# Kernel tuning notes

Measured on AMD Instinct MI355X. Metric: run time of the kernel, lower is better.

The kernel has to match this reference:

```python
import jax, jax.numpy as jnp
import numpy as np

KS = (10, 25, 50, 100)  # numbers of highest-scored tiles to average (eval mode averages over all)
CLAMP = 1e4


def setup_inputs() -> dict:
    key = jax.random.key(0)
    k1, k2, k3, k4, k5, k6, k7 = jax.random.split(key, 7)
    B, C, N, H, O = 8, 2048, 8000, 256, 1000
    x = jax.random.normal(k1, (B, C, N), dtype=jnp.float32)
    # Conv1d(kernel=1) weights == [out, in] matrices
    W0 = jax.random.normal(k2, (H, C), dtype=jnp.float32) * (1.0 / np.sqrt(C))
    b0 = jax.random.normal(k3, (H,), dtype=jnp.float32) * 0.01
    W1 = jax.random.normal(k4, (H, H), dtype=jnp.float32) * (1.0 / np.sqrt(H))
    b1 = jax.random.normal(k5, (H,), dtype=jnp.float32) * 0.01
    W2 = jax.random.normal(k6, (O, H), dtype=jnp.float32) * (1.0 / np.sqrt(H))
    b2 = jax.random.normal(k7, (O,), dtype=jnp.float32) * 0.01
    return {"x": x, "W0": W0, "b0": b0, "W1": W1, "b1": b1, "W2": W2, "b2": b2}


def reference(x, W0, b0, W1, b1, W2, b2):
    # x: [B, C, N] tile features. Eval-mode dropout is identity.
    # mask: tile is 'real' if its max feature > 0 (padding tiles are all-zero)
    mask = (jnp.max(x, axis=1, keepdims=True) > 0).astype(x.dtype)  # [B,1,N]
    # 1x1 conv stack (Conv1d kernel=1 == per-tile matmul)
    h = jnp.einsum('hc,bcn->bhn', W0, x) + b0[None, :, None]
    h = jnp.clip(jax.nn.relu(h), -CLAMP, CLAMP)
    h = jnp.einsum('hg,bgn->bhn', W1, h) + b1[None, :, None]
    h = jnp.clip(jax.nn.relu(h), -CLAMP, CLAMP)
    y = jnp.einsum('oh,bhn->bon', W2, h) + b2[None, :, None]  # [B,O,N]
    y = y * mask
    # top-kmax once (sorted descending); top-k for smaller k is a prefix slice
    kmax = max(KS)
    t, _ = jax.lax.top_k(y, kmax)  # [B,O,kmax]
    pred = jnp.zeros(y.shape[:2], dtype=y.dtype)  # [B,O]
    inv = 1.0 / len(KS)
    for k in KS:
        num = jnp.sum(t[:, :, :k] * mask[:, :, :k], axis=2)  # [B,O]
        den = jnp.sum(mask[:, :, :k], axis=2)                 # [B,1]
        pred = pred + (num / den) * inv
    return pred
```

## Files before the change

### kernel.cpp

```cpp
#include <hip/hip_runtime.h>
#include <hip/hip_bf16.h>
#include <stdint.h>

typedef __bf16 bf16;
typedef __bf16 bf16x8 __attribute__((ext_vector_type(8)));
typedef __bf16 bf16x4 __attribute__((ext_vector_type(4)));
typedef float  floatx4 __attribute__((ext_vector_type(4)));
typedef unsigned int uint32;

#define B_  8
#define C_  2048
#define N_  8000
#define H_  256
#define O_  1000
#define OP_ 1024

__device__ __forceinline__ void gll16(const void* g, void* l) {
  __builtin_amdgcn_global_load_lds((const __attribute__((address_space(1))) void*)g,
                                   (__attribute__((address_space(3))) void*)l, 16, 0, 0);
}

__global__ __launch_bounds__(256) void castw(const float* __restrict__ W0,
                                             const float* __restrict__ W1,
                                             const float* __restrict__ W2,
                                             bf16* __restrict__ W0b,
                                             bf16* __restrict__ W1b,
                                             bf16* __restrict__ W2b) {
  int idx = blockIdx.x * 256 + threadIdx.x;
  if (idx < 524288) {
    W0b[idx] = (bf16)W0[idx];
  } else if (idx < 524288 + 65536) {
    int i = idx - 524288;
    W1b[i] = (bf16)W1[i];
  } else {
    int i = idx - (524288 + 65536);
    int o = i >> 8, k = i & 255;
    W2b[i] = (o < O_) ? (bf16)W2[o * 256 + k] : (bf16)0.0f;
  }
}

__global__ __launch_bounds__(256) void gemm1(const float* __restrict__ x,
                                             const bf16* __restrict__ W0b,
                                             const float* __restrict__ bias0,
                                             bf16* __restrict__ h1T,
                                             float* __restrict__ maskb) {
  __shared__ union {
    struct { bf16 A[H_ * 32]; bf16 Bt[64 * 40]; } st;
    bf16 HT[64 * 264];
  } sm;
  __shared__ float sbias[256];
  __shared__ uint32 nflag[64];

  const int tid  = threadIdx.x;
  const int wave = tid >> 6, lane = tid & 63;
  const int l16  = lane & 15, l4 = lane >> 4;
  const int n0   = blockIdx.x * 64;
  const int b    = blockIdx.y;

  sbias[tid] = bias0[tid];
  if (tid < 64) nflag[tid] = 0;

  const int kp = tid >> 4;
  const int n4 = (tid & 15) * 4;
  const float* xbase = x + (size_t)b * C_ * N_ + n0 + n4;

  floatx4 acc[4][4];
  #pragma unroll
  for (int i = 0; i < 4; ++i)
    #pragma unroll
    for (int j = 0; j < 4; ++j)
      acc[i][j] = floatx4{0.f, 0.f, 0.f, 0.f};

  uint32 fl = 0;

  for (int k0 = 0; k0 < C_; k0 += 32) {
    #pragma unroll
    for (int i = 0; i < 4; ++i) {
      int c = i * 256 + tid;
      gll16(W0b + (size_t)(c >> 2) * C_ + k0 + (c & 3) * 8, &sm.st.A[c * 8]);
    }
    const float* xr = xbase + (size_t)(k0 + 2 * kp) * N_;
    float4 q0 = *(const float4*)xr;
    float4 q1 = *(const float4*)(xr + N_);
    float a0[4] = {q0.x, q0.y, q0.z, q0.w};
    float a1[4] = {q1.x, q1.y, q1.z, q1.w};
    uint32* bw = (uint32*)sm.st.Bt;
    #pragma unroll
    for (int i = 0; i < 4; ++i) {
      if (a0[i] > 0.f || a1[i] > 0.f) fl |= (1u << i);
      union { bf16 h[2]; uint32 u; } p;
      p.h[0] = (bf16)a0[i];
      p.h[1] = (bf16)a1[i];
      bw[(n4 + i) * 20 + kp] = p.u;
    }
    __syncthreads();

    bf16x8 af[4], bfr[4];
    #pragma unroll
    for (int mt = 0; mt < 4; ++mt)
      af[mt] = *(const bf16x8*)&sm.st.A[(wave * 64 + mt * 16 + l16) * 32 + l4 * 8];
    #pragma unroll
    for (int nt = 0; nt < 4; ++nt)
      bfr[nt] = *(const bf16x8*)&sm.st.Bt[(nt * 16 + l16) * 40 + l4 * 8];
    #pragma unroll
    for (int mt = 0; mt < 4; ++mt)
      #pragma unroll
      for (int nt = 0; nt < 4; ++nt)
        acc[mt][nt] = __builtin_amdgcn_mfma_f32_16x16x32_bf16(af[mt], bfr[nt], acc[mt][nt], 0, 0, 0);
    __syncthreads();
  }

  #pragma unroll
  for (int i = 0; i < 4; ++i)
    if (fl & (1u << i)) atomicOr(&nflag[n4 + i], 1u);
  __syncthreads();
  if (tid < 64) maskb[(size_t)b * N_ + n0 + tid] = nflag[tid] ? 1.f : 0.f;

  #pragma unroll
  for (int mt = 0; mt < 4; ++mt) {
    int m0 = wave * 64 + mt * 16 + l4 * 4;
    #pragma unroll
    for (int nt = 0; nt < 4; ++nt) {
      int n = nt * 16 + l16;
      bf16x4 hv;
      #pragma unroll
      for (int r = 0; r < 4; ++r) {
        float v = acc[mt][nt][r] + sbias[m0 + r];
        v = fminf(fmaxf(v, 0.f), 1.0e4f);
        hv[r] = (bf16)v;
      }
      *(bf16x4*)&sm.HT[n * 264 + m0] = hv;
    }
  }
  __syncthreads();
  {
    int n = tid >> 2, q = tid & 3;
    const char* src = (const char*)&sm.HT[n * 264 + q * 64];
    bf16* dst = h1T + ((size_t)b * N_ + n0 + n) * H_ + q * 64;
    #pragma unroll
    for (int j = 0; j < 8; ++j)
      *(uint4*)((char*)dst + j * 16) = *(const uint4*)(src + j * 16);
  }
}

template <int OUTL>
__global__ __launch_bounds__(256) void gemmA(const bf16* __restrict__ A,
                                             const float* __restrict__ bias, int biasLim,
                                             const bf16* __restrict__ Bt,
                                             bf16* __restrict__ outp) {
  __shared__ union {
    struct { bf16 A[256 * 32]; bf16 Bs[64 * 32]; } st;
    bf16 HT[64 * 264];
    bf16 YT[256 * 72];
  } sm;
  __shared__ float sbias[256];

  const int tid  = threadIdx.x;
  const int wave = tid >> 6, lane = tid & 63;
  const int l16  = lane & 15, l4 = lane >> 4;
  const int n0   = blockIdx.x * 64;
  const int mb   = blockIdx.y;
  const int b    = blockIdx.z;
  const int m0g  = mb * 256;

  { int og = m0g + tid; sbias[tid] = (og < biasLim) ? bias[og] : 0.f; }

  floatx4 acc[4][4];
  #pragma unroll
  for (int i = 0; i < 4; ++i)
    #pragma unroll
    for (int j = 0; j < 4; ++j)
      acc[i][j] = floatx4{0.f, 0.f, 0.f, 0.f};

  const bf16* Bbase = Bt + ((size_t)b * N_ + n0) * 256;

  for (int k0 = 0; k0 < 256; k0 += 32) {
    #pragma unroll
    for (int i = 0; i < 4; ++i) {
      int c = i * 256 + tid;
      gll16(A + (size_t)(m0g + (c >> 2)) * 256 + k0 + (c & 3) * 8, &sm.st.A[c * 8]);
    }
    gll16(Bbase + (size_t)(tid >> 2) * 256 + k0 + (tid & 3) * 8, &sm.st.Bs[tid * 8]);
    __syncthreads();

    bf16x8 af[4], bfr[4];
    #pragma unroll
    for (int mt = 0; mt < 4; ++mt)
      af[mt] = *(const bf16x8*)&sm.st.A[(wave * 64 + mt * 16 + l16) * 32 + l4 * 8];
    #pragma unroll
    for (int nt = 0; nt < 4; ++nt)
      bfr[nt] = *(const bf16x8*)&sm.st.Bs[(nt * 16 + l16) * 32 + l4 * 8];
    #pragma unroll
    for (int mt = 0; mt < 4; ++mt)
      #pragma unroll
      for (int nt = 0; nt < 4; ++nt)
        acc[mt][nt] = __builtin_amdgcn_mfma_f32_16x16x32_bf16(af[mt], bfr[nt], acc[mt][nt], 0, 0, 0);
    __syncthreads();
  }

  if constexpr (!OUTL) {
    #pragma unroll
    for (int mt = 0; mt < 4; ++mt) {
      int m0 = wave * 64 + mt * 16 + l4 * 4;
      #pragma unroll
      for (int nt = 0; nt < 4; ++nt) {
        int n = nt * 16 + l16;
        bf16x4 hv;
        #pragma unroll
        for (int r = 0; r < 4; ++r) {
          float v = acc[mt][nt][r] + sbias[m0 + r];
          v = fminf(fmaxf(v, 0.f), 1.0e4f);
          hv[r] = (bf16)v;
        }
        *(bf16x4*)&sm.HT[n * 264 + m0] = hv;
      }
    }
    __syncthreads();
    int n = tid >> 2, q = tid & 3;
    const char* src = (const char*)&sm.HT[n * 264 + q * 64];
    bf16* dst = outp + ((size_t)b * N_ + n0 + n) * H_ + q * 64;
    #pragma unroll
    for (int j = 0; j < 8; ++j)
      *(uint4*)((char*)dst + j * 16) = *(const uint4*)(src + j * 16);
  } else {
    #pragma unroll
    for (int mt = 0; mt < 4; ++mt) {
      int m0 = wave * 64 + mt * 16 + l4 * 4;
      #pragma unroll
      for (int nt = 0; nt < 4; ++nt) {
        int n = nt * 16 + l16;
        #pragma unroll
        for (int r = 0; r < 4; ++r) {
          float v = acc[mt][nt][r] + sbias[m0 + r];
          sm.YT[(m0 + r) * 72 + n] = (bf16)v;
        }
      }
    }
    __syncthreads();
    bf16* dst = outp + ((size_t)b * OP_ + m0g + tid) * N_ + n0;
    const char* src = (const char*)&sm.YT[tid * 72];
    #pragma unroll
    for (int j = 0; j < 8; ++j)
      *(uint4*)((char*)dst + j * 16) = *(const uint4*)(src + j * 16);
  }
}

__global__ __launch_bounds__(256) void topk(const bf16* __restrict__ y,
                                            const float* __restrict__ maskb,
                                            float* __restrict__ out) {
  __shared__ uint32 keys[4096];
  __shared__ uint32 cand[128];
  __shared__ float  sval[128];
  __shared__ float  m100[128];
  __shared__ int    redw[4][3];
  __shared__ int    gcnt;

  const int tid  = threadIdx.x;
  const int wave = tid >> 6, lane = tid & 63;
  const int o = blockIdx.x, b = blockIdx.y;

  const uint32* yw = (const uint32*)(y + ((size_t)b * OP_ + o) * N_);
  const float*  mr = maskb + (size_t)b * N_;

  if (tid < 128) m100[tid] = (tid < 100) ? mr[tid] : 0.f;
  if (tid == 0) gcnt = 0;

  #pragma unroll
  for (int i = 0; i < 16; ++i) {
    int w = i * 256 + tid;
    uint32 kk = 0;
    if (w < 4000) {
      uint32 v = yw[w];
      float2 mm = *(const float2*)(mr + 2 * w);
      uint32 b0 = v & 0xffffu, b1 = v >> 16;
      if (mm.x == 0.f) b0 = 0u;
      if (mm.y == 0.f) b1 = 0u;
      uint32 k0 = (b0 & 0x8000u) ? (~b0 & 0xffffu) : (b0 | 0x8000u);
      uint32 k1 = (b1 & 0x8000u) ? (~b1 & 0xffffu) : (b1 | 0x8000u);
      kk = k0 | (k1 << 16);
    }
    keys[w] = kk;
  }
  __syncthreads();

  uint32 prefix = 0;
  for (int shift = 14; shift >= 0; shift -= 2) {
    uint32 t1 = prefix | (1u << shift);
    uint32 t2 = prefix | (2u << shift);
    uint32 t3 = prefix | (3u << shift);
    int c1 = 0, c2 = 0, c3 = 0;
    #pragma unroll
    for (int i = 0; i < 16; ++i) {
      uint32 w = keys[i * 256 + tid];
      uint32 k0 = w & 0xffffu, k1 = w >> 16;
      c1 += (k0 >= t1) + (k1 >= t1);
      c2 += (k0 >= t2) + (k1 >= t2);
      c3 += (k0 >= t3) + (k1 >= t3);
    }
    #pragma unroll
    for (int off = 32; off > 0; off >>= 1) {
      c1 += __shfl_down(c1, off);
      c2 += __shfl_down(c2, off);
      c3 += __shfl_down(c3, off);
    }
    if (lane == 0) { redw[wave][0] = c1; redw[wave][1] = c2; redw[wave][2] = c3; }
    __syncthreads();
    int n1 = redw[0][0] + redw[1][0] + redw[2][0] + redw[3][0];
    int n2 = redw[0][1] + redw[1][1] + redw[2][1] + redw[3][1];
    int n3 = redw[0][2] + redw[1][2] + redw[2][2] + redw[3][2];
    if (n3 >= 100)      prefix = t3;
    else if (n2 >= 100) prefix = t2;
    else if (n1 >= 100) prefix = t1;
    __syncthreads();
  }

  #pragma unroll
  for (int i = 0; i < 16; ++i) {
    uint32 w = keys[i * 256 + tid];
    uint32 k0 = w & 0xffffu, k1 = w >> 16;
    if (k0 > prefix) { int p = atomicAdd(&gcnt, 1); cand[p] = k0; }
    if (k1 > prefix) { int p = atomicAdd(&gcnt, 1); cand[p] = k1; }
  }
  __syncthreads();
  int cg = gcnt;
  if (tid >= cg && tid < 100) cand[tid] = prefix;
  __syncthreads();

  if (tid < 100) {
    uint32 ci = cand[tid];
    int rank = 0;
    for (int j = 0; j < 100; ++j) {
      uint32 cj = cand[j];
      rank += (cj > ci) || (cj == ci && j < tid);
    }
    uint32 bb = (ci & 0x8000u) ? (ci & 0x7fffu) : (~ci & 0xffffu);
    sval[rank] = __uint_as_float(bb << 16);
  }
  __syncthreads();

  if (tid == 0) {
    const int KSv[4] = {10, 25, 50, 100};
    float num = 0.f, den = 0.f, pred = 0.f;
    int ki = 0;
    for (int j = 0; j < 100; ++j) {
      num += sval[j] * m100[j];
      den += m100[j];
      if (j + 1 == KSv[ki]) { pred += 0.25f * num / den; ++ki; }
    }
    out[(size_t)b * O_ + o] = pred;
  }
}

extern "C" void kernel_launch(void* const* d_in, const int* in_sizes, int n_in,
                              void* d_out, int out_size, void* d_ws, size_t ws_size,
                              hipStream_t stream) {
  const float* x  = (const float*)d_in[0];
  const float* W0 = (const float*)d_in[1];
  const float* b0 = (const float*)d_in[2];
  const float* W1 = (const float*)d_in[3];
  const float* b1 = (const float*)d_in[4];
  const float* W2 = (const float*)d_in[5];
  const float* b2 = (const float*)d_in[6];
  float* out = (float*)d_out;

  char* ws = (char*)d_ws;
  bf16*  W0b  = (bf16*)(ws + 0);
  bf16*  W1b  = (bf16*)(ws + 1048576);
  bf16*  W2b  = (bf16*)(ws + 1179648);
  float* mk   = (float*)(ws + 1703936);
  bf16*  h1T  = (bf16*)(ws + 1959936);
  bf16*  h2T  = (bf16*)(ws + 34727936);
  bf16*  yb   = (bf16*)(ws + 67495936);

  castw<<<3328, 256, 0, stream>>>(W0, W1, W2, W0b, W1b, W2b);
  gemm1<<<dim3(125, 8), 256, 0, stream>>>(x, W0b, b0, h1T, mk);
  gemmA<0><<<dim3(125, 1, 8), 256, 0, stream>>>(W1b, b1, H_, h1T, h2T);
  gemmA<1><<<dim3(125, 4, 8), 256, 0, stream>>>(W2b, b2, O_, h2T, yb);
  topk<<<dim3(1000, 8), 256, 0, stream>>>(yb, mk, out);
}
```

Baseline: 1.008 ms.

## Fold mask into GEMM epilogue and run top-k as a single-wave register radix select

```diff
diff --git a/kernel.cpp b/kernel.cpp
--- a/kernel.cpp
+++ b/kernel.cpp
@@ -147,6 +147,7 @@
 __global__ __launch_bounds__(256) void gemmA(const bf16* __restrict__ A,
                                              const float* __restrict__ bias, int biasLim,
                                              const bf16* __restrict__ Bt,
+                                             const float* __restrict__ mk,
                                              bf16* __restrict__ outp) {
   __shared__ union {
     struct { bf16 A[256 * 32]; bf16 Bs[64 * 32]; } st;
@@ -154,6 +155,7 @@
     bf16 YT[256 * 72];
   } sm;
   __shared__ float sbias[256];
+  __shared__ float smk[64];
 
   const int tid  = threadIdx.x;
   const int wave = tid >> 6, lane = tid & 63;
@@ -164,6 +166,7 @@
   const int m0g  = mb * 256;
 
   { int og = m0g + tid; sbias[tid] = (og < biasLim) ? bias[og] : 0.f; }
+  if (OUTL && tid < 64) smk[tid] = mk[(size_t)b * N_ + n0 + tid];
 
   floatx4 acc[4][4];
   #pragma unroll
@@ -229,9 +232,10 @@
       #pragma unroll
       for (int nt = 0; nt < 4; ++nt) {
         int n = nt * 16 + l16;
+        float m = smk[n];
         #pragma unroll
         for (int r = 0; r < 4; ++r) {
-          float v = acc[mt][nt][r] + sbias[m0 + r];
+          float v = (acc[mt][nt][r] + sbias[m0 + r]) * m;
           sm.YT[(m0 + r) * 72 + n] = (bf16)v;
         }
       }
@@ -245,100 +249,86 @@
   }
 }
 
-__global__ __launch_bounds__(256) void topk(const bf16* __restrict__ y,
-                                            const float* __restrict__ maskb,
-                                            float* __restrict__ out) {
-  __shared__ uint32 keys[4096];
+__global__ __launch_bounds__(64) void topk(const bf16* __restrict__ y,
+                                           const float* __restrict__ maskb,
+                                           float* __restrict__ out) {
   __shared__ uint32 cand[128];
   __shared__ float  sval[128];
-  __shared__ float  m100[128];
-  __shared__ int    redw[4][3];
+  __shared__ float  m100[100];
   __shared__ int    gcnt;
 
-  const int tid  = threadIdx.x;
-  const int wave = tid >> 6, lane = tid & 63;
+  const int lane = threadIdx.x;
   const int o = blockIdx.x, b = blockIdx.y;
 
   const uint32* yw = (const uint32*)(y + ((size_t)b * OP_ + o) * N_);
   const float*  mr = maskb + (size_t)b * N_;
 
-  if (tid < 128) m100[tid] = (tid < 100) ? mr[tid] : 0.f;
-  if (tid == 0) gcnt = 0;
-
+  if (lane == 0) gcnt = 0;
+  m100[lane] = mr[lane];
+  if (lane < 36) m100[64 + lane] = mr[64 + lane];
+
+  uint32 khi[64], klo[64];
   #pragma unroll
   for (int i = 0; i < 16; ++i) {
-    int w = i * 256 + tid;
-    uint32 kk = 0;
-    if (w < 4000) {
-      uint32 v = yw[w];
-      float2 mm = *(const float2*)(mr + 2 * w);
-      uint32 b0 = v & 0xffffu, b1 = v >> 16;
-      if (mm.x == 0.f) b0 = 0u;
-      if (mm.y == 0.f) b1 = 0u;
-      uint32 k0 = (b0 & 0x8000u) ? (~b0 & 0xffffu) : (b0 | 0x8000u);
-      uint32 k1 = (b1 & 0x8000u) ? (~b1 & 0xffffu) : (b1 | 0x8000u);
-      kk = k0 | (k1 << 16);
-    }
-    keys[w] = kk;
-  }
-  __syncthreads();
+    int base = i * 256 + lane * 4;
+    bool real = (base < 4000);
+    uint4 v = make_uint4(0u, 0u, 0u, 0u);
+    if (real) v = *(const uint4*)(yw + base);
+    uint32 ww[4] = {v.x, v.y, v.z, v.w};
+    #pragma unroll
+    for (int j = 0; j < 4; ++j) {
+      uint32 w = ww[j];
+      uint32 sgn = w & 0x80008000u;
+      uint32 mskk = 0x80008000u | (sgn - (sgn >> 15));
+      uint32 k = w ^ mskk;
+      if (!real) k = 0u;
+      khi[i * 4 + j] = k;
+      klo[i * 4 + j] = k << 16;
+    }
+  }
 
   uint32 prefix = 0;
-  for (int shift = 14; shift >= 0; shift -= 2) {
-    uint32 t1 = prefix | (1u << shift);
-    uint32 t2 = prefix | (2u << shift);
-    uint32 t3 = prefix | (3u << shift);
-    int c1 = 0, c2 = 0, c3 = 0;
-    #pragma unroll
-    for (int i = 0; i < 16; ++i) {
-      uint32 w = keys[i * 256 + tid];
-      uint32 k0 = w & 0xffffu, k1 = w >> 16;
-      c1 += (k0 >= t1) + (k1 >= t1);
-      c2 += (k0 >= t2) + (k1 >= t2);
-      c3 += (k0 >= t3) + (k1 >= t3);
-    }
-    #pragma unroll
-    for (int off = 32; off > 0; off >>= 1) {
-      c1 += __shfl_down(c1, off);
-      c2 += __shfl_down(c2, off);
-      c3 += __shfl_down(c3, off);
-    }
-    if (lane == 0) { redw[wave][0] = c1; redw[wave][1] = c2; redw[wave][2] = c3; }
-    __syncthreads();
-    int n1 = redw[0][0] + redw[1][0] + redw[2][0] + redw[3][0];
-    int n2 = redw[0][1] + redw[1][1] + redw[2][1] + redw[3][1];
-    int n3 = redw[0][2] + redw[1][2] + redw[2][2] + redw[3][2];
-    if (n3 >= 100)      prefix = t3;
-    else if (n2 >= 100) prefix = t2;
-    else if (n1 >= 100) prefix = t1;
-    __syncthreads();
-  }
-
-  #pragma unroll
-  for (int i = 0; i < 16; ++i) {
-    uint32 w = keys[i * 256 + tid];
-    uint32 k0 = w & 0xffffu, k1 = w >> 16;
-    if (k0 > prefix) { int p = atomicAdd(&gcnt, 1); cand[p] = k0; }
-    if (k1 > prefix) { int p = atomicAdd(&gcnt, 1); cand[p] = k1; }
+  #pragma unroll 1
+  for (int bit = 15; bit >= 0; --bit) {
+    uint32 T16 = (prefix | (1u << bit)) << 16;
+    int c = 0, d = 0;
+    #pragma unroll
+    for (int r = 0; r < 64; ++r) {
+      c += (khi[r] >= T16);
+      d += (klo[r] >= T16);
+    }
+    c += d;
+    #pragma unroll
+    for (int m = 1; m < 64; m <<= 1) c += __shfl_xor(c, m, 64);
+    if (c >= 100) prefix |= (1u << bit);
+  }
+
+  #pragma unroll
+  for (int r = 0; r < 64; ++r) {
+    uint32 h = khi[r] >> 16;
+    uint32 l = khi[r] & 0xffffu;
+    if (h > prefix) { int p = atomicAdd(&gcnt, 1); cand[p] = h; }
+    if (l > prefix) { int p = atomicAdd(&gcnt, 1); cand[p] = l; }
   }
   __syncthreads();
   int cg = gcnt;
-  if (tid >= cg && tid < 100) cand[tid] = prefix;
-  __syncthreads();
-
-  if (tid < 100) {
-    uint32 ci = cand[tid];
+  for (int idx = lane; idx < 100; idx += 64)
+    if (idx >= cg) cand[idx] = prefix;
+  __syncthreads();
+
+  for (int idx = lane; idx < 100; idx += 64) {
+    uint32 ci = cand[idx];
     int rank = 0;
     for (int j = 0; j < 100; ++j) {
       uint32 cj = cand[j];
-      rank += (cj > ci) || (cj == ci && j < tid);
+      rank += (cj > ci) || (cj == ci && j < idx);
     }
     uint32 bb = (ci & 0x8000u) ? (ci & 0x7fffu) : (~ci & 0xffffu);
     sval[rank] = __uint_as_float(bb << 16);
   }
   __syncthreads();
 
-  if (tid == 0) {
+  if (lane == 0) {
     const int KSv[4] = {10, 25, 50, 100};
     float num = 0.f, den = 0.f, pred = 0.f;
     int ki = 0;
@@ -374,7 +364,7 @@
 
   castw<<<3328, 256, 0, stream>>>(W0, W1, W2, W0b, W1b, W2b);
   gemm1<<<dim3(125, 8), 256, 0, stream>>>(x, W0b, b0, h1T, mk);
-  gemmA<0><<<dim3(125, 1, 8), 256, 0, stream>>>(W1b, b1, H_, h1T, h2T);
-  gemmA<1><<<dim3(125, 4, 8), 256, 0, stream>>>(W2b, b2, O_, h2T, yb);
-  topk<<<dim3(1000, 8), 256, 0, stream>>>(yb, mk, out);
-}
+  gemmA<0><<<dim3(125, 1, 8), 256, 0, stream>>>(W1b, b1, H_, h1T, nullptr, h2T);
+  gemmA<1><<<dim3(125, 4, 8), 256, 0, stream>>>(W2b, b2, O_, h2T, mk, yb);
+  topk<<<dim3(1000, 8), 64, 0, stream>>>(yb, mk, out);
+}
```

After: 985.7 us. -2.2%, faster.
